# Kernel tuning notes

Measured on AMD Instinct MI355X. Metric: run time of the kernel, lower is better.

The kernel has to match this reference:

```python
import jax, jax.numpy as jnp
import numpy as np

D_MODEL = 1024
N_HEADS = 16
HEAD_DIM = D_MODEL // N_HEADS


def setup_inputs() -> dict:
    key = jax.random.key(0)
    ks = jax.random.split(key, 9)
    B, S = 2, 2048
    s = 1.0 / np.sqrt(D_MODEL)
    return {
        "x": jax.random.normal(ks[0], (B, S, D_MODEL), dtype=jnp.float32),
        "Wq": jax.random.normal(ks[1], (D_MODEL, D_MODEL), dtype=jnp.float32) * s,
        "bq": jnp.zeros((D_MODEL,), dtype=jnp.float32),
        "Wk": jax.random.normal(ks[2], (D_MODEL, D_MODEL), dtype=jnp.float32) * s,
        "bk": jnp.zeros((D_MODEL,), dtype=jnp.float32),
        "Wv": jax.random.normal(ks[3], (D_MODEL, D_MODEL), dtype=jnp.float32) * s,
        "bv": jnp.zeros((D_MODEL,), dtype=jnp.float32),
        "Wo": jax.random.normal(ks[4], (D_MODEL, D_MODEL), dtype=jnp.float32) * s,
        "bo": jnp.zeros((D_MODEL,), dtype=jnp.float32),
    }


def _rope_emb(seq_len, dtype):
    # inv_freq over even dims of head_dim; emb = cat(freqs, freqs)
    inv_freq = 1.0 / (10000.0 ** (jnp.arange(0, HEAD_DIM, 2, dtype=jnp.float32) / HEAD_DIM))
    t = jnp.arange(seq_len, dtype=jnp.float32)
    freqs = t[:, None] * inv_freq[None, :]          # [S, head_dim/2]
    emb = jnp.concatenate([freqs, freqs], axis=-1)  # [S, head_dim]
    return emb.astype(dtype)[None, None, :, :]       # [1,1,S,head_dim]


def _rotate_half(x):
    x1, x2 = jnp.split(x, 2, axis=-1)
    return jnp.concatenate([-x2, x1], axis=-1)


def _apply_rope(x, emb):
    return x * jnp.cos(emb) + _rotate_half(x) * jnp.sin(emb)


def reference(x, Wq, bq, Wk, bk, Wv, bv, Wo, bo):
    B, S, _ = x.shape
    # projections (torch Linear: x @ W.T + b; here W is stored already as [in,out])
    q = (x @ Wq + bq).reshape(B, S, N_HEADS, HEAD_DIM).transpose(0, 2, 1, 3)
    k = (x @ Wk + bk).reshape(B, S, N_HEADS, HEAD_DIM).transpose(0, 2, 1, 3)
    v = (x @ Wv + bv).reshape(B, S, N_HEADS, HEAD_DIM).transpose(0, 2, 1, 3)
    emb = _rope_emb(S, x.dtype)
    q = _apply_rope(q, emb)
    k = _apply_rope(k, emb)
    scores = jnp.einsum('bhqd,bhkd->bhqk', q, k) / jnp.sqrt(jnp.asarray(HEAD_DIM, x.dtype))
    attn = jax.nn.softmax(scores, axis=-1)
    out = jnp.einsum('bhqk,bhkd->bhqd', attn, v)
    out = out.transpose(0, 2, 1, 3).reshape(B, S, D_MODEL)
    return out @ Wo + bo
```

## Files before the change

### kernel.cpp

```cpp
#include <hip/hip_runtime.h>
#include <hip/hip_bf16.h>
#include <math.h>

#define SEQ 2048
#define DM 1024
#define NH 16
#define HD 64
#define NBH 32
#define MTOT 4096

typedef __attribute__((ext_vector_type(8))) short short8;
typedef __attribute__((ext_vector_type(4))) float floatx4;
typedef __attribute__((ext_vector_type(8))) unsigned short u16x8;
typedef __attribute__((ext_vector_type(4))) unsigned short u16x4;

__device__ __forceinline__ unsigned short f2bf(float f) {
    unsigned int u = __float_as_uint(f);
    u += 0x7FFFu + ((u >> 16) & 1u);
    return (unsigned short)(u >> 16);
}
__device__ __forceinline__ float bf2f(unsigned short h) {
    unsigned int u = (unsigned int)h << 16;
    return __uint_as_float(u);
}

#define AS1C const __attribute__((address_space(1))) void*
#define AS3  __attribute__((address_space(3))) void*

#define QSCALE 0.18033688011112042f

__global__ __launch_bounds__(256) void cvt_xw_kernel(
    const float* __restrict__ x, unsigned short* __restrict__ xb,
    const float* __restrict__ Wq, const float* __restrict__ Wk,
    const float* __restrict__ Wv, const float* __restrict__ Wo,
    unsigned short* __restrict__ Wt)
{
    if (blockIdx.x < 2048) {
        size_t base = ((size_t)blockIdx.x * 256 + threadIdx.x) * 8;
        float4 a = *(const float4*)(x + base);
        float4 b = *(const float4*)(x + base + 4);
        u16x8 o;
        o[0]=f2bf(a.x); o[1]=f2bf(a.y); o[2]=f2bf(a.z); o[3]=f2bf(a.w);
        o[4]=f2bf(b.x); o[5]=f2bf(b.y); o[6]=f2bf(b.z); o[7]=f2bf(b.w);
        *(u16x8*)(xb + base) = o;
        return;
    }
    __shared__ float Ls[64][65];
    const int bid = blockIdx.x - 2048;
    const int z = bid >> 8;
    const float* src = (z==0) ? Wq : (z==1) ? Wk : (z==2) ? Wv : Wo;
    unsigned short* dst = Wt + (size_t)z * DM * DM;
    const int tid = threadIdx.x;
    const int k0 = (bid & 15) * 64, n0 = ((bid >> 4) & 15) * 64;

    int r = tid >> 2, cseg = (tid & 3) * 16;
    #pragma unroll
    for (int e = 0; e < 4; ++e) {
        float4 v = *(const float4*)(src + (size_t)(k0 + r) * DM + n0 + cseg + e*4);
        Ls[r][cseg+e*4+0] = v.x; Ls[r][cseg+e*4+1] = v.y;
        Ls[r][cseg+e*4+2] = v.z; Ls[r][cseg+e*4+3] = v.w;
    }
    __syncthreads();
    int n = tid >> 2, kseg = (tid & 3) * 16;
    #pragma unroll
    for (int half = 0; half < 2; ++half) {
        u16x8 o;
        #pragma unroll
        for (int e = 0; e < 8; ++e) o[e] = f2bf(Ls[kseg + half*8 + e][n]);
        *(u16x8*)(dst + (size_t)(n0 + n) * DM + k0 + kseg + half*8) = o;
    }
}

#define GEMM_CORE(A_, Bt_, m0_, n0_)                                          \
    const int tid = threadIdx.x;                                              \
    const int wave = tid >> 6, lane = tid & 63;                               \
    const int quad = lane >> 4, l16 = lane & 15;                              \
    const int mh = (wave & 1) * 64, nh = (wave >> 1) * 64;                    \
    floatx4 acc[4][4];                                                        \
    _Pragma("unroll")                                                         \
    for (int i = 0; i < 4; ++i)                                               \
        _Pragma("unroll")                                                     \
        for (int j = 0; j < 4; ++j) acc[i][j] = (floatx4){0.f,0.f,0.f,0.f};   \
    {                                                                         \
        const int srow = wave*32 + (lane>>2);                                 \
        const int scol = (lane & 3) * 8;                                      \
        const unsigned short* ga = A_ + (size_t)(m0_ + srow)*DM + scol;       \
        const unsigned short* gb = Bt_ + (size_t)(n0_ + srow)*DM + scol;      \
        char* lA = (char*)As; char* lB = (char*)Bs;                           \
        for (int k0 = 0; k0 < DM; k0 += 32) {                                 \
            __syncthreads();                                                  \
            _Pragma("unroll")                                                 \
            for (int u = 0; u < 2; ++u) {                                     \
                __builtin_amdgcn_global_load_lds(                             \
                    (AS1C)(ga + (size_t)u*16*DM + k0),                        \
                    (AS3)(lA + (wave*32 + u*16)*64), 16, 0, 0);               \
                __builtin_amdgcn_global_load_lds(                             \
                    (AS1C)(gb + (size_t)u*16*DM + k0),                        \
                    (AS3)(lB + (wave*32 + u*16)*64), 16, 0, 0);               \
            }                                                                 \
            __syncthreads();                                                  \
            short8 af[4], bf[4];                                              \
            _Pragma("unroll")                                                 \
            for (int t = 0; t < 4; ++t) {                                     \
                af[t] = *(const short8*)&As[(mh + t*16 + l16)*32 + quad*8];   \
                bf[t] = *(const short8*)&Bs[(nh + t*16 + l16)*32 + quad*8];   \
            }                                                                 \
            _Pragma("unroll")                                                 \
            for (int mt = 0; mt < 4; ++mt)                                    \
                _Pragma("unroll")                                             \
                for (int nt = 0; nt < 4; ++nt)                                \
                    acc[mt][nt] = __builtin_amdgcn_mfma_f32_16x16x32_bf16(    \
                        af[mt], bf[nt], acc[mt][nt], 0, 0, 0);                \
        }                                                                     \
    }

__global__ __launch_bounds__(256, 3) void qkv_gemm_kernel(
    const unsigned short* __restrict__ xb, const unsigned short* __restrict__ Wt,
    const float* __restrict__ bq, const float* __restrict__ bk,
    const float* __restrict__ bv,
    unsigned short* __restrict__ qb, unsigned short* __restrict__ kb,
    unsigned short* __restrict__ vtg)
{
    __shared__ unsigned short As[128*32];
    __shared__ unsigned short Bs[128*32];
    const int z = blockIdx.z;
    const unsigned short* Bt = Wt + (size_t)z * DM * DM;
    const float* bias = (z==0) ? bq : (z==1) ? bk : bv;
    const int m0 = blockIdx.x * 128, n0 = blockIdx.y * 128;

    GEMM_CORE(xb, Bt, m0, n0)

    float bb[4];
    #pragma unroll
    for (int nt = 0; nt < 4; ++nt) bb[nt] = bias[n0 + nh + nt*16 + l16];

    if (z == 2) {
        unsigned short* Tw = (wave & 1) ? Bs : As;
        const int b = m0 >> 11;
        const int bufsel = tid >> 7, nl = tid & 127;
        const int ng = n0 + nl, hh = ng >> 6, dhh = ng & 63;
        unsigned short* vrow = vtg + ((size_t)((b*NH + hh)*HD + dhh))*SEQ;
        #pragma unroll
        for (int t = 0; t < 4; ++t) {
            __syncthreads();
            #pragma unroll
            for (int nt = 0; nt < 4; ++nt)
                #pragma unroll
                for (int r = 0; r < 4; ++r)
                    Tw[(nh + nt*16 + l16)*24 + quad*4 + r] =
                        f2bf(acc[t][nt][r] + bb[nt]);
            __syncthreads();
            const unsigned short* T2 = bufsel ? Bs : As;
            int sbase = (m0 & 2047) + bufsel*64 + t*16;
            int t32 = (sbase >> 4) & 1;
            int sb32 = sbase & ~31;
            #pragma unroll
            for (int gq = 0; gq < 4; ++gq) {
                u16x4 v4 = *(const u16x4*)&T2[nl*24 + gq*4];
                *(u16x4*)(vrow + sb32 + gq*8 + t32*4) = v4;
            }
        }
    } else {
        unsigned short* outh = (z==0) ? qb : kb;
        const float scl = (z == 0) ? QSCALE : 1.0f;
        const int h = (n0 + nh) >> 6;
        float inv0 = __expf(-(float)l16        * 0.28782313662425572f);
        float inv1 = __expf(-(float)(l16 + 16) * 0.28782313662425572f);
        #pragma unroll
        for (int mt = 0; mt < 4; ++mt)
            #pragma unroll
            for (int r = 0; r < 4; ++r) {
                int m = m0 + mh + mt*16 + quad*4 + r;
                int b = m >> 11, s = m & (SEQ-1);
                float s0, c0, s1, c1;
                __sincosf((float)s * inv0, &s0, &c0);
                __sincosf((float)s * inv1, &s1, &c1);
                float a0 = acc[mt][0][r] + bb[0];
                float a1 = acc[mt][1][r] + bb[1];
                float a2 = acc[mt][2][r] + bb[2];
                float a3 = acc[mt][3][r] + bb[3];
                u16x4 o;
                o[0] = f2bf((a0*c0 - a2*s0) * scl);
                o[1] = f2bf((a1*c1 - a3*s1) * scl);
                o[2] = f2bf((a2*c0 + a0*s0) * scl);
                o[3] = f2bf((a3*c1 + a1*s1) * scl);
                *(u16x4*)(outh + ((size_t)((b*NH + h)*SEQ + s))*HD + 4*l16) = o;
            }
    }
}

__global__ __launch_bounds__(256, 3) void out_gemm_kernel(
    const unsigned short* __restrict__ ctxb, const unsigned short* __restrict__ Wto,
    const float* __restrict__ bo, float* __restrict__ outf)
{
    __shared__ unsigned short As[128*32];
    __shared__ unsigned short Bs[128*32];
    const int m0 = blockIdx.x * 128, n0 = blockIdx.y * 128;

    GEMM_CORE(ctxb, Wto, m0, n0)

    float bb[4];
    #pragma unroll
    for (int nt = 0; nt < 4; ++nt) bb[nt] = bo[n0 + nh + nt*16 + l16];
    #pragma unroll
    for (int mt = 0; mt < 4; ++mt)
        #pragma unroll
        for (int r = 0; r < 4; ++r) {
            int m = m0 + mh + mt*16 + quad*4 + r;
            #pragma unroll
            for (int nt = 0; nt < 4; ++nt) {
                int n = n0 + nh + nt*16 + l16;
                outf[(size_t)m*DM + n] = acc[mt][nt][r] + bb[nt];
            }
        }
}

__global__ __launch_bounds__(256, 2) void attn_mfma_kernel(
    const unsigned short* __restrict__ Q, const unsigned short* __restrict__ K,
    const unsigned short* __restrict__ Vtg,
    unsigned short* __restrict__ Opart, float* __restrict__ Lpart)
{
    __shared__ unsigned short Ks[2*128*32];
    __shared__ unsigned short Vt[4*64*32];

    const int tid  = threadIdx.x;
    const int wave = tid >> 6, lane = tid & 63;
    const int quad = lane >> 4, l16 = lane & 15;
    const int bh   = blockIdx.x & 31;
    const int qt   = (blockIdx.x >> 5) & 15;
    const int half = blockIdx.x >> 9;

    const unsigned short* Qb = Q + (size_t)bh * SEQ * HD;
    const unsigned short* Kb = K + (size_t)bh * SEQ * HD + (size_t)half*1024*HD;
    const unsigned short* Vb = Vtg + (size_t)bh * HD * SEQ + half*1024;

    short8 qf[2][2];
    #pragma unroll
    for (int qg = 0; qg < 2; ++qg) {
        const unsigned short* qrow =
            Qb + (size_t)(qt*128 + wave*32 + qg*16 + l16)*HD;
        qf[qg][0] = *(const short8*)(qrow + quad*8);
        qf[qg][1] = *(const short8*)(qrow + 32 + quad*8);
    }

    const unsigned short* gsrc[8];
    char* ldst[8];
    int step;
    if (wave < 2) {
        #pragma unroll
        for (int u = 0; u < 8; ++u) {
            int G = u*128 + wave*64 + lane;
            int gl = G & 3, key = (G >> 2) & 127, s = G >> 9;
            gsrc[u] = Kb + (size_t)key*HD + s*32 + (gl ^ ((key>>2)&3))*8;
            ldst[u] = (char*)Ks + G*16;
        }
        step = 128*HD;
    } else {
        #pragma unroll
        for (int u = 0; u < 8; ++u) {
            int G = u*128 + (wave-2)*64 + lane;
            int gl = G & 3, d = (G >> 2) & 63, g = G >> 8;
            gsrc[u] = Vb + (size_t)d*SEQ + g*32 + (gl ^ ((d>>2)&3))*8;
            ldst[u] = (char*)Vt + G*16;
        }
        step = 128;
    }

    float l_p[2] = {0.f, 0.f};
    floatx4 Oacc[2][4];
    #pragma unroll
    for (int qg = 0; qg < 2; ++qg)
        #pragma unroll
        for (int dt = 0; dt < 4; ++dt) Oacc[qg][dt] = (floatx4){0.f,0.f,0.f,0.f};

    const int swz = (quad ^ (l16 >> 2)) * 8;

    for (int kt = 0; kt < 8; ++kt) {
        __syncthreads();
        #pragma unroll
        for (int u = 0; u < 8; ++u)
            __builtin_amdgcn_global_load_lds((AS1C)gsrc[u], (AS3)ldst[u], 16, 0, 0);
        #pragma unroll
        for (int u = 0; u < 8; ++u) gsrc[u] += step;
        __syncthreads();

        #pragma unroll
        for (int g = 0; g < 4; ++g) {
            floatx4 Sc[2][2];
            #pragma unroll
            for (int t = 0; t < 2; ++t)
                #pragma unroll
                for (int qg = 0; qg < 2; ++qg) Sc[t][qg] = (floatx4){0.f,0.f,0.f,0.f};
            #pragma unroll
            for (int t = 0; t < 2; ++t) {
                const int c = g*2 + t;
                #pragma unroll
                for (int s = 0; s < 2; ++s) {
                    short8 af = *(const short8*)&Ks[s*4096 + (c*16 + l16)*32 + swz];
                    #pragma unroll
                    for (int qg = 0; qg < 2; ++qg)
                        Sc[t][qg] = __builtin_amdgcn_mfma_f32_16x16x32_bf16(
                            af, qf[qg][s], Sc[t][qg], 0, 0, 0);
                }
            }
            short8 a8[2];
            #pragma unroll
            for (int qg = 0; qg < 2; ++qg) {
                float p[8];
                #pragma unroll
                for (int t = 0; t < 2; ++t)
                    #pragma unroll
                    for (int r = 0; r < 4; ++r) p[t*4+r] = exp2f(Sc[t][qg][r]);
                l_p[qg] += ((p[0]+p[1]) + (p[2]+p[3])) + ((p[4]+p[5]) + (p[6]+p[7]));
                u16x8 av;
                #pragma unroll
                for (int e = 0; e < 4; ++e) {
                    __hip_bfloat162 w = __float22bfloat162_rn(make_float2(p[2*e], p[2*e+1]));
                    unsigned int uu; __builtin_memcpy(&uu, &w, 4);
                    av[2*e]   = (unsigned short)(uu & 0xFFFF);
                    av[2*e+1] = (unsigned short)(uu >> 16);
                }
                __builtin_memcpy(&a8[qg], &av, 16);
            }
            #pragma unroll
            for (int dt = 0; dt < 4; ++dt) {
                short8 bf = *(const short8*)&Vt[g*2048 + (dt*16 + l16)*32 + swz];
                #pragma unroll
                for (int qg = 0; qg < 2; ++qg)
                    Oacc[qg][dt] = __builtin_amdgcn_mfma_f32_16x16x32_bf16(
                        a8[qg], bf, Oacc[qg][dt], 0, 0, 0);
            }
        }
    }

    #pragma unroll
    for (int qg = 0; qg < 2; ++qg) {
        l_p[qg] += __shfl_xor(l_p[qg], 16);
        l_p[qg] += __shfl_xor(l_p[qg], 32);
    }

    size_t obase = (((size_t)((half*32 + bh)*16 + qt))*128)*64;
    #pragma unroll
    for (int qg = 0; qg < 2; ++qg) {
        #pragma unroll
        for (int r = 0; r < 4; ++r) {
            int ql = wave*32 + qg*16 + quad*4 + r;
            unsigned short* dst = Opart + obase + (size_t)ql*64;
            #pragma unroll
            for (int dt = 0; dt < 4; ++dt)
                dst[dt*16 + l16] = f2bf(Oacc[qg][dt][r]);
        }
        if (quad == 0)
            Lpart[((size_t)(half*32 + bh))*SEQ + qt*128 + wave*32 + qg*16 + l16]
                = l_p[qg];
    }
}

__global__ __launch_bounds__(256) void attn_combine_kernel(
    const unsigned short* __restrict__ Opart, const float* __restrict__ Lpart,
    unsigned short* __restrict__ ctxb)
{
    const size_t HS = (size_t)32*16*128*64;
    int idx = blockIdx.x*256 + threadIdx.x;
    int oct = idx & 7;
    int q   = (idx >> 3) & (SEQ-1);
    int bh  = idx >> 14;
    int qt = q >> 7, ql = q & 127;
    size_t pbase = ((((size_t)(bh*16 + qt))*128 + ql)*64) + oct*8;
    u16x8 o1 = *(const u16x8*)(Opart + pbase);
    u16x8 o2 = *(const u16x8*)(Opart + HS + pbase);
    float l = Lpart[(size_t)bh*SEQ + q] + Lpart[(size_t)32*SEQ + bh*SEQ + q];
    float inv = 1.0f / l;
    u16x8 o;
    #pragma unroll
    for (int e = 0; e < 8; ++e)
        o[e] = f2bf((bf2f(o1[e]) + bf2f(o2[e])) * inv);
    int b = bh >> 4, h = bh & 15;
    *(u16x8*)(ctxb + ((size_t)(b*SEQ + q))*DM + h*HD + oct*8) = o;
}

extern "C" void kernel_launch(void* const* d_in, const int* in_sizes, int n_in,
                              void* d_out, int out_size, void* d_ws, size_t ws_size,
                              hipStream_t stream) {
    const float* x  = (const float*)d_in[0];
    const float* Wq = (const float*)d_in[1];
    const float* bq = (const float*)d_in[2];
    const float* Wk = (const float*)d_in[3];
    const float* bk = (const float*)d_in[4];
    const float* Wv = (const float*)d_in[5];
    const float* bv = (const float*)d_in[6];
    const float* Wo = (const float*)d_in[7];
    const float* bo = (const float*)d_in[8];
    float* out = (float*)d_out;

    char* ws = (char*)d_ws;
    unsigned short* xb   = (unsigned short*)(ws);
    unsigned short* Wt   = (unsigned short*)(ws +  8u*1024*1024);
    unsigned short* qb   = (unsigned short*)(ws + 16u*1024*1024);
    unsigned short* kb   = (unsigned short*)(ws + 24u*1024*1024);
    unsigned short* vtg  = (unsigned short*)(ws + 32u*1024*1024);
    unsigned short* ctxb = (unsigned short*)(ws + 40u*1024*1024);
    unsigned short* Op   = (unsigned short*)(ws + 48u*1024*1024);
    float*          Lp   = (float*)(ws);

    cvt_xw_kernel<<<3072, 256, 0, stream>>>(x, xb, Wq, Wk, Wv, Wo, Wt);

    qkv_gemm_kernel<<<dim3(MTOT/128, DM/128, 3), 256, 0, stream>>>(
        xb, Wt, bq, bk, bv, qb, kb, vtg);

    attn_mfma_kernel<<<1024, 256, 0, stream>>>(qb, kb, vtg, Op, Lp);
    attn_combine_kernel<<<2048, 256, 0, stream>>>(Op, Lp, ctxb);

    out_gemm_kernel<<<dim3(MTOT/128, DM/128), 256, 0, stream>>>(
        ctxb, Wt + (size_t)3*DM*DM, bo, out);
    (void)in_sizes; (void)n_in; (void)out_size; (void)ws_size;
}
```

Baseline: 203.7 us.

## Fuse split-K attention combine into attention kernel via atomic counter; retile out GEMM

Removes the separate combine kernel. Each attention block atomically bumps a per-tile counter, and the second finisher merges its register accumulator with the other half's partial output and normalizer, writing ctx directly. The output GEMM moves to 64x128 tiles with its own inline loop, and the attention kernel's launch bound and bf16 packing also change. This cuts one launch and one full read pass of the partials, at the cost of a memset, fences, and higher register pressure from the raised occupancy hint.

```diff
diff --git a/kernel.cpp b/kernel.cpp
--- a/kernel.cpp
+++ b/kernel.cpp
@@ -189,39 +189,78 @@
     }
 }
 
-__global__ __launch_bounds__(256, 3) void out_gemm_kernel(
+__global__ __launch_bounds__(256, 2) void out_gemm_kernel(
     const unsigned short* __restrict__ ctxb, const unsigned short* __restrict__ Wto,
     const float* __restrict__ bo, float* __restrict__ outf)
 {
-    __shared__ unsigned short As[128*32];
+    __shared__ unsigned short As[64*32];
     __shared__ unsigned short Bs[128*32];
-    const int m0 = blockIdx.x * 128, n0 = blockIdx.y * 128;
-
-    GEMM_CORE(ctxb, Wto, m0, n0)
-
-    float bb[4];
-    #pragma unroll
-    for (int nt = 0; nt < 4; ++nt) bb[nt] = bo[n0 + nh + nt*16 + l16];
+    const int tid = threadIdx.x;
+    const int wave = tid >> 6, lane = tid & 63;
+    const int quad = lane >> 4, l16 = lane & 15;
+    const int m0 = blockIdx.x * 64, n0 = blockIdx.y * 128;
+    const int nw = wave * 32;
+
+    floatx4 acc[4][2];
+    #pragma unroll
+    for (int i = 0; i < 4; ++i)
+        #pragma unroll
+        for (int j = 0; j < 2; ++j) acc[i][j] = (floatx4){0.f,0.f,0.f,0.f};
+
+    const int srow = lane >> 2;
+    const int scol = (lane & 3) * 8;
+    const unsigned short* ga = ctxb + (size_t)(m0 + wave*16 + srow)*DM + scol;
+    const unsigned short* gb = Wto + (size_t)(n0 + wave*16 + srow)*DM + scol;
+    char* lA = (char*)As; char* lB = (char*)Bs;
+
+    for (int k0 = 0; k0 < DM; k0 += 32) {
+        __syncthreads();
+        __builtin_amdgcn_global_load_lds((AS1C)(ga + k0),
+                                         (AS3)(lA + wave*1024), 16, 0, 0);
+        #pragma unroll
+        for (int u = 0; u < 2; ++u)
+            __builtin_amdgcn_global_load_lds((AS1C)(gb + (size_t)u*64*DM + k0),
+                                             (AS3)(lB + u*4096 + wave*1024), 16, 0, 0);
+        __syncthreads();
+        short8 af[4], bf[2];
+        #pragma unroll
+        for (int t = 0; t < 4; ++t)
+            af[t] = *(const short8*)&As[(t*16 + l16)*32 + quad*8];
+        #pragma unroll
+        for (int t = 0; t < 2; ++t)
+            bf[t] = *(const short8*)&Bs[(nw + t*16 + l16)*32 + quad*8];
+        #pragma unroll
+        for (int mt = 0; mt < 4; ++mt)
+            #pragma unroll
+            for (int nt = 0; nt < 2; ++nt)
+                acc[mt][nt] = __builtin_amdgcn_mfma_f32_16x16x32_bf16(
+                    af[mt], bf[nt], acc[mt][nt], 0, 0, 0);
+    }
+
+    float bb[2];
+    #pragma unroll
+    for (int nt = 0; nt < 2; ++nt) bb[nt] = bo[n0 + nw + nt*16 + l16];
     #pragma unroll
     for (int mt = 0; mt < 4; ++mt)
         #pragma unroll
         for (int r = 0; r < 4; ++r) {
-            int m = m0 + mh + mt*16 + quad*4 + r;
-            #pragma unroll
-            for (int nt = 0; nt < 4; ++nt) {
-                int n = n0 + nh + nt*16 + l16;
-                outf[(size_t)m*DM + n] = acc[mt][nt][r] + bb[nt];
-            }
-        }
-}
-
-__global__ __launch_bounds__(256, 2) void attn_mfma_kernel(
+            int m = m0 + mt*16 + quad*4 + r;
+            #pragma unroll
+            for (int nt = 0; nt < 2; ++nt)
+                outf[(size_t)m*DM + n0 + nw + nt*16 + l16] = acc[mt][nt][r] + bb[nt];
+        }
+}
+
+__global__ __launch_bounds__(256, 4) void attn_mfma_kernel(
     const unsigned short* __restrict__ Q, const unsigned short* __restrict__ K,
     const unsigned short* __restrict__ Vtg,
-    unsigned short* __restrict__ Opart, float* __restrict__ Lpart)
+    unsigned short* __restrict__ Opart, float* __restrict__ Lpart,
+    int* __restrict__ cnt, unsigned short* __restrict__ ctxb)
 {
     __shared__ unsigned short Ks[2*128*32];
     __shared__ unsigned short Vt[4*64*32];
+    __shared__ float Lred[4][32];
+    __shared__ int amSecond;
 
     const int tid  = threadIdx.x;
     const int wave = tid >> 6, lane = tid & 63;
@@ -312,15 +351,13 @@
                     #pragma unroll
                     for (int r = 0; r < 4; ++r) p[t*4+r] = exp2f(Sc[t][qg][r]);
                 l_p[qg] += ((p[0]+p[1]) + (p[2]+p[3])) + ((p[4]+p[5]) + (p[6]+p[7]));
-                u16x8 av;
+                unsigned int pk[4];
                 #pragma unroll
                 for (int e = 0; e < 4; ++e) {
                     __hip_bfloat162 w = __float22bfloat162_rn(make_float2(p[2*e], p[2*e+1]));
-                    unsigned int uu; __builtin_memcpy(&uu, &w, 4);
-                    av[2*e]   = (unsigned short)(uu & 0xFFFF);
-                    av[2*e+1] = (unsigned short)(uu >> 16);
+                    __builtin_memcpy(&pk[e], &w, 4);
                 }
-                __builtin_memcpy(&a8[qg], &av, 16);
+                __builtin_memcpy(&a8[qg], pk, 16);
             }
             #pragma unroll
             for (int dt = 0; dt < 4; ++dt) {
@@ -337,6 +374,7 @@
     for (int qg = 0; qg < 2; ++qg) {
         l_p[qg] += __shfl_xor(l_p[qg], 16);
         l_p[qg] += __shfl_xor(l_p[qg], 32);
+        Lred[wave][qg*16 + l16] = l_p[qg];
     }
 
     size_t obase = (((size_t)((half*32 + bh)*16 + qt))*128)*64;
@@ -354,29 +392,32 @@
             Lpart[((size_t)(half*32 + bh))*SEQ + qt*128 + wave*32 + qg*16 + l16]
                 = l_p[qg];
     }
-}
-
-__global__ __launch_bounds__(256) void attn_combine_kernel(
-    const unsigned short* __restrict__ Opart, const float* __restrict__ Lpart,
-    unsigned short* __restrict__ ctxb)
-{
-    const size_t HS = (size_t)32*16*128*64;
-    int idx = blockIdx.x*256 + threadIdx.x;
-    int oct = idx & 7;
-    int q   = (idx >> 3) & (SEQ-1);
-    int bh  = idx >> 14;
-    int qt = q >> 7, ql = q & 127;
-    size_t pbase = ((((size_t)(bh*16 + qt))*128 + ql)*64) + oct*8;
-    u16x8 o1 = *(const u16x8*)(Opart + pbase);
-    u16x8 o2 = *(const u16x8*)(Opart + HS + pbase);
-    float l = Lpart[(size_t)bh*SEQ + q] + Lpart[(size_t)32*SEQ + bh*SEQ + q];
-    float inv = 1.0f / l;
-    u16x8 o;
-    #pragma unroll
-    for (int e = 0; e < 8; ++e)
-        o[e] = f2bf((bf2f(o1[e]) + bf2f(o2[e])) * inv);
-    int b = bh >> 4, h = bh & 15;
-    *(u16x8*)(ctxb + ((size_t)(b*SEQ + q))*DM + h*HD + oct*8) = o;
+
+    __threadfence();
+    if (tid == 0) amSecond = atomicAdd(&cnt[blockIdx.x & 511], 1);
+    __syncthreads();
+    if (amSecond == 1) {
+        __threadfence();
+        const int oh = 1 - half;
+        size_t obase2 = (((size_t)((oh*32 + bh)*16 + qt))*128)*64;
+        const float* Lp2 = Lpart + ((size_t)(oh*32 + bh))*SEQ + qt*128;
+        int b = bh >> 4, hh = bh & 15;
+        #pragma unroll
+        for (int qg = 0; qg < 2; ++qg)
+            #pragma unroll
+            for (int r = 0; r < 4; ++r) {
+                int ql = wave*32 + qg*16 + quad*4 + r;
+                float lt = Lred[wave][qg*16 + quad*4 + r] + Lp2[ql];
+                float inv = 1.0f / lt;
+                const unsigned short* src = Opart + obase2 + (size_t)ql*64;
+                unsigned short* dst =
+                    ctxb + ((size_t)(b*SEQ + qt*128 + ql))*DM + hh*HD;
+                #pragma unroll
+                for (int dt = 0; dt < 4; ++dt)
+                    dst[dt*16 + l16] =
+                        f2bf((Oacc[qg][dt][r] + bf2f(src[dt*16 + l16])) * inv);
+            }
+    }
 }
 
 extern "C" void kernel_launch(void* const* d_in, const int* in_sizes, int n_in,
@@ -402,16 +443,18 @@
     unsigned short* ctxb = (unsigned short*)(ws + 40u*1024*1024);
     unsigned short* Op   = (unsigned short*)(ws + 48u*1024*1024);
     float*          Lp   = (float*)(ws);
+    int*            cnt  = (int*)(ws + 512u*1024);
 
     cvt_xw_kernel<<<3072, 256, 0, stream>>>(x, xb, Wq, Wk, Wv, Wo, Wt);
 
     qkv_gemm_kernel<<<dim3(MTOT/128, DM/128, 3), 256, 0, stream>>>(
         xb, Wt, bq, bk, bv, qb, kb, vtg);
 
-    attn_mfma_kernel<<<1024, 256, 0, stream>>>(qb, kb, vtg, Op, Lp);
-    attn_combine_kernel<<<2048, 256, 0, stream>>>(Op, Lp, ctxb);
-
-    out_gemm_kernel<<<dim3(MTOT/128, DM/128), 256, 0, stream>>>(
+    hipMemsetAsync(cnt, 0, 512 * sizeof(int), stream);
+
+    attn_mfma_kernel<<<1024, 256, 0, stream>>>(qb, kb, vtg, Op, Lp, cnt, ctxb);
+
+    out_gemm_kernel<<<dim3(MTOT/64, DM/128), 256, 0, stream>>>(
         ctxb, Wt + (size_t)3*DM*DM, bo, out);
     (void)in_sizes; (void)n_in; (void)out_size; (void)ws_size;
 }
```

New measurement: 460.3 us. 126% more time.
